# Kernel tuning notes

Measured on AMD Instinct MI355X. Metric: run time of the kernel, lower is better.

## Reference

```python
import jax, jax.numpy as jnp
import numpy as np

V = 50257
D = 512
T = 1024


def setup_inputs() -> dict:
    key = jax.random.key(0)
    ks = jax.random.split(key, 12)
    si = (2.0 / (V + D)) ** 0.5   # xavier-ish scale for input matrices
    sh = (1.0 / D) ** 0.5         # scale for recurrent matrices
    so = (2.0 / (V + D)) ** 0.5
    return {
        "idx": jax.random.randint(ks[0], (T,), 0, V, dtype=jnp.int32),
        "W_ii": jax.random.normal(ks[1], (D, V), jnp.float32) * si,
        "W_if": jax.random.normal(ks[2], (D, V), jnp.float32) * si,
        "W_io": jax.random.normal(ks[3], (D, V), jnp.float32) * si,
        "W_ig": jax.random.normal(ks[4], (D, V), jnp.float32) * si,
        "W_hi": jax.random.normal(ks[5], (D, D), jnp.float32) * sh,
        "W_hf": jax.random.normal(ks[6], (D, D), jnp.float32) * sh,
        "W_ho": jax.random.normal(ks[7], (D, D), jnp.float32) * sh,
        "W_hg": jax.random.normal(ks[8], (D, D), jnp.float32) * sh,
        "b_i": jnp.zeros((D,), jnp.float32),
        "b_f": jnp.ones((D,), jnp.float32),
        "b_o": jnp.zeros((D,), jnp.float32),
        "b_g": jnp.zeros((D,), jnp.float32),
        "W_out": jax.random.normal(ks[9], (V, D), jnp.float32) * so,
        "b_out": jnp.zeros((V,), jnp.float32),
    }


def reference(idx, W_ii, W_if, W_io, W_ig, W_hi, W_hf, W_ho, W_hg,
              b_i, b_f, b_o, b_g, W_out, b_out):
    # One-hot @ W.T == column gather: W[:, tok]. Dropout is identity (eval mode).
    dims = W_hi.shape[0]

    def step(carry, tok):
        h, c = carry
        i = jax.nn.sigmoid(W_ii[:, tok] + b_i + W_hi @ h)
        f = jax.nn.sigmoid(W_if[:, tok] + b_f + W_hf @ h)
        o = jax.nn.sigmoid(W_io[:, tok] + b_o + W_ho @ h)
        g = jnp.tanh(W_ig[:, tok] + b_g + W_hg @ h)
        c_new = f * c + i * g
        h_new = o * jnp.tanh(c_new)
        logits = W_out @ h_new + b_out          # [V]
        return (h_new, c_new), jax.nn.log_softmax(logits)

    h0 = jnp.zeros((dims,), W_hi.dtype)
    c0 = jnp.zeros((dims,), W_hi.dtype)
    (h, c), log_probs = jax.lax.scan(step, (h0, c0), idx)
    return log_probs, h, c  # log_probs: [T, V]
```

## Files before the change

### kernel.cpp

```cpp
#include <hip/hip_runtime.h>
#include <hip/hip_bf16.h>

#define VV 50257
#define DD 512
#define TT 1024
#define VPADN 50304
#define NBR 64
#define WCB 128
#define PSTR 400

typedef __bf16 bf16;
typedef __attribute__((ext_vector_type(8))) __bf16 bf16x8;
typedef __attribute__((ext_vector_type(4))) __bf16 bf16x4;
typedef __attribute__((ext_vector_type(4))) float f32x4;

__device__ __forceinline__ void gload_lds16(const void* g, void* l) {
  __builtin_amdgcn_global_load_lds(
      (__attribute__((address_space(1))) void*)(void*)g,
      (__attribute__((address_space(3))) void*)l, 16, 0, 0);
}

__global__ __launch_bounds__(512) __attribute__((amdgpu_waves_per_eu(2, 2)))
void recur_fused_kernel(
    const int* __restrict__ idx,
    const float* __restrict__ Wii, const float* __restrict__ Wif,
    const float* __restrict__ Wio, const float* __restrict__ Wig,
    const float* __restrict__ Whi, const float* __restrict__ Whf,
    const float* __restrict__ Who, const float* __restrict__ Whg,
    const float* __restrict__ bi, const float* __restrict__ bfv,
    const float* __restrict__ bo, const float* __restrict__ bg,
    const float* __restrict__ Wout,
    unsigned long long* __restrict__ Hpack, bf16* __restrict__ Hbf,
    bf16* __restrict__ Wbf, float* __restrict__ out_tail) {
  __shared__ float hsh[2][DD];
  __shared__ int idxs[TT];
  const int b = blockIdx.x, tid = threadIdx.x;

  if (b >= NBR) {
    const int wb = b - NBR;
    const size_t nch = (size_t)VPADN * DD / 4;
    for (size_t i = (size_t)wb * 512 + tid; i < nch; i += (size_t)WCB * 512) {
      size_t e = i << 2;
      bf16x4 o;
      if ((e >> 9) < VV) {
        f32x4 x = *(const f32x4*)&Wout[e];
        o[0] = (bf16)x[0]; o[1] = (bf16)x[1]; o[2] = (bf16)x[2]; o[3] = (bf16)x[3];
      } else {
        o[0] = o[1] = o[2] = o[3] = (bf16)0.f;
      }
      *(bf16x4*)&Wbf[e] = o;
    }
    return;
  }

  idxs[tid] = idx[tid];
  idxs[tid + 512] = idx[tid + 512];

  const int lane = tid & 63, w = tid >> 6;
  const int hd = (b << 3) + w;

  f32x4 wr0[4], wr1[4];
  {
    #pragma unroll
    for (int gg = 0; gg < 4; ++gg) {
      const float* Wg = (gg == 0) ? Whi : (gg == 1) ? Whf : (gg == 2) ? Who : Whg;
      wr0[gg] = *(const f32x4*)&Wg[(size_t)hd*DD + (lane << 2)];
      wr1[gg] = *(const f32x4*)&Wg[(size_t)hd*DD + 256 + (lane << 2)];
    }
  }
  #pragma unroll
  for (int gg = 0; gg < 4; ++gg) {
    asm volatile("" : "+v"(wr0[gg]));
    asm volatile("" : "+v"(wr1[gg]));
  }

  const float* wxp = nullptr;
  float bias = 0.f;
  if (lane < 4) {
    const float* Wx = (lane == 0) ? Wii : (lane == 1) ? Wif : (lane == 2) ? Wio : Wig;
    const float* bx = (lane == 0) ? bi : (lane == 1) ? bfv : (lane == 2) ? bo : bg;
    wxp = &Wx[(size_t)hd * VV];
    bias = bx[hd];
  }
  float c = 0.f, hout = 0.f;
  __syncthreads();

  for (int t = 0; t < TT; ++t) {
    float xv = 0.f;
    if (lane < 4) xv = wxp[idxs[t]] + bias;

    float* hb = hsh[t & 1];
    if (t > 0) {
      __builtin_amdgcn_s_sleep(8);
      const unsigned long long* src = &Hpack[(size_t)(t-1)*DD + tid];
      unsigned long long v;
      do {
        asm volatile("global_load_dwordx2 %0, %1, off sc1\n\t"
                     "s_waitcnt vmcnt(0)"
                     : "=v"(v) : "v"(src) : "memory");
      } while (__builtin_expect((unsigned)(v >> 32) != (unsigned)t, 0));
      hb[tid] = __uint_as_float((unsigned)v);
    } else {
      hb[tid] = 0.f;
    }
    __syncthreads();

    const f32x4 h0 = *(const f32x4*)&hb[lane << 2];
    const f32x4 h1 = *(const f32x4*)&hb[256 + (lane << 2)];
    f32x4 m0 = wr0[0]*h0 + wr1[0]*h1;
    f32x4 m1 = wr0[1]*h0 + wr1[1]*h1;
    f32x4 m2 = wr0[2]*h0 + wr1[2]*h1;
    f32x4 m3 = wr0[3]*h0 + wr1[3]*h1;
    float a0 = m0[0]+m0[1]+m0[2]+m0[3];
    float a1 = m1[0]+m1[1]+m1[2]+m1[3];
    float a2 = m2[0]+m2[1]+m2[2]+m2[3];
    float a3 = m3[0]+m3[1]+m3[2]+m3[3];
    #pragma unroll
    for (int mask = 1; mask < 64; mask <<= 1) {
      a0 += __shfl_xor(a0, mask);
      a1 += __shfl_xor(a1, mask);
      a2 += __shfl_xor(a2, mask);
      a3 += __shfl_xor(a3, mask);
    }

    float myacc = (lane == 0) ? a0 : (lane == 1) ? a1 : (lane == 2) ? a2 : a3;
    float pre = myacc + xv;
    bool isg = (lane == 3);
    float e1 = __expf(isg ? -2.f * pre : -pre);
    float rr = 1.f / (1.f + e1);
    float act = isg ? (2.f * rr - 1.f) : rr;

    float ia = __shfl(act, 0);
    float fa = __shfl(act, 1);
    float oa = __shfl(act, 2);
    float ga = __shfl(act, 3);

    if (lane == 0) {
      c = fa * c + ia * ga;
      float e2 = __expf(-2.f * c);
      float th = 2.f / (1.f + e2) - 1.f;
      hout = oa * th;
      unsigned long long pk =
          ((unsigned long long)(unsigned)(t + 1) << 32) |
          (unsigned long long)__float_as_uint(hout);
      __hip_atomic_store(&Hpack[(size_t)t*DD + hd], pk, __ATOMIC_RELAXED,
                         __HIP_MEMORY_SCOPE_AGENT);
      Hbf[(size_t)t*DD + hd] = (bf16)hout;
      if (t == TT - 1) { out_tail[hd] = hout; out_tail[DD + hd] = c; }
    }
  }
}

__global__ __launch_bounds__(256, 2) void gemm_kernel(
    const bf16* __restrict__ A, const bf16* __restrict__ B,
    const float* __restrict__ bout, float* __restrict__ Cout,
    float* __restrict__ Pmax, float* __restrict__ Psum) {
  __shared__ bf16 As[128*32];
  __shared__ bf16 Bs[128*32];
  __shared__ float Cs[4][16][72];
  __shared__ float partm[2][2][16];
  __shared__ float parts[2][2][16];
  const int tid = threadIdx.x;
  const int nb = blockIdx.x;
  const int n0 = nb * 128, m0 = blockIdx.y * 128;
  const int w = tid >> 6, l = tid & 63;
  const int wr = w >> 1, wc = w & 1;
  f32x4 acc[4][4] = {};

  for (int k0 = 0; k0 < DD; k0 += 32) {
    #pragma unroll
    for (int c = 0; c < 2; ++c) {
      int j = c*256 + tid;
      int row = j >> 2, kc = (j & 3) << 3;
      gload_lds16(&A[(size_t)(m0 + row)*DD + k0 + kc], (char*)As + (c*4096 + w*1024));
      gload_lds16(&B[(size_t)(n0 + row)*DD + k0 + kc], (char*)Bs + (c*4096 + w*1024));
    }
    __syncthreads();
    bf16x8 af[4], bfr[4];
    #pragma unroll
    for (int mi = 0; mi < 4; ++mi)
      af[mi] = *(const bf16x8*)&As[(wr*64 + mi*16 + (l & 15))*32 + (l >> 4)*8];
    #pragma unroll
    for (int ni = 0; ni < 4; ++ni)
      bfr[ni] = *(const bf16x8*)&Bs[(wc*64 + ni*16 + (l & 15))*32 + (l >> 4)*8];
    #pragma unroll
    for (int mi = 0; mi < 4; ++mi)
      #pragma unroll
      for (int ni = 0; ni < 4; ++ni)
        acc[mi][ni] = __builtin_amdgcn_mfma_f32_16x16x32_bf16(af[mi], bfr[ni], acc[mi][ni], 0, 0, 0);
    __syncthreads();
  }

  float bbv[4];
  bool colok[4];
  #pragma unroll
  for (int ni = 0; ni < 4; ++ni) {
    int col = n0 + wc*64 + ni*16 + (l & 15);
    colok[ni] = (col < VV);
    bbv[ni] = colok[ni] ? bout[col] : 0.f;
  }

  #pragma unroll
  for (int mi = 0; mi < 4; ++mi) {
    #pragma unroll
    for (int ni = 0; ni < 4; ++ni)
      #pragma unroll
      for (int r = 0; r < 4; ++r)
        Cs[w][(l >> 4)*4 + r][ni*16 + (l & 15)] = acc[mi][ni][r] + bbv[ni];

    #pragma unroll
    for (int r = 0; r < 4; ++r) {
      float v0 = colok[0] ? acc[mi][0][r] + bbv[0] : -1e30f;
      float v1 = colok[1] ? acc[mi][1][r] + bbv[1] : -1e30f;
      float v2 = colok[2] ? acc[mi][2][r] + bbv[2] : -1e30f;
      float v3 = colok[3] ? acc[mi][3][r] + bbv[3] : -1e30f;
      float pm = fmaxf(fmaxf(v0, v1), fmaxf(v2, v3));
      #pragma unroll
      for (int mk = 1; mk < 16; mk <<= 1) pm = fmaxf(pm, __shfl_xor(pm, mk));
      float ps = __expf(v0 - pm) + __expf(v1 - pm) + __expf(v2 - pm) + __expf(v3 - pm);
      #pragma unroll
      for (int mk = 1; mk < 16; mk <<= 1) ps += __shfl_xor(ps, mk);
      if ((l & 15) == 0) {
        partm[wr][wc][(l >> 4)*4 + r] = pm;
        parts[wr][wc][(l >> 4)*4 + r] = ps;
      }
    }
    __syncthreads();
    if (tid < 32) {
      int wr2 = tid >> 4, row16 = tid & 15;
      float ma = partm[wr2][0][row16], mb = partm[wr2][1][row16];
      float M = fmaxf(ma, mb);
      float S = parts[wr2][0][row16]*__expf(ma - M) + parts[wr2][1][row16]*__expf(mb - M);
      int gr = m0 + wr2*64 + mi*16 + row16;
      Pmax[(size_t)gr*PSTR + nb] = M;
      Psum[(size_t)gr*PSTR + nb] = S;
    }

    const int rbase = m0 + wr*64 + mi*16;
    #pragma unroll
    for (int i = 0; i < 4; ++i) {
      int idx2 = i*64 + l;
      int row = idx2 >> 4, quad = idx2 & 15;
      int col = n0 + wc*64 + quad*4;
      f32x4 v = *(const f32x4*)&Cs[w][row][quad*4];
      float* dst = &Cout[(size_t)(rbase + row)*VV + col];
      if (col + 3 < VV) {
        asm volatile("global_store_dwordx4 %0, %1, off"
                     :: "v"(dst), "v"(v) : "memory");
      } else {
        #pragma unroll
        for (int e = 0; e < 4; ++e)
          if (col + e < VV) dst[e] = v[e];
      }
    }
    __syncthreads();
  }
}

__global__ __launch_bounds__(512) void lsm_kernel(float* __restrict__ logits,
                                                  const float* __restrict__ Pmax,
                                                  const float* __restrict__ Psum) {
  const int t = blockIdx.x, tid = threadIdx.x;
  float* row = logits + (size_t)t*VV;

  float m = -1e30f, s = 0.f;
  if (tid < 393) {
    m = Pmax[(size_t)t*PSTR + tid];
    s = Psum[(size_t)t*PSTR + tid];
  }
  #pragma unroll
  for (int mask = 1; mask < 64; mask <<= 1) {
    float om = __shfl_xor(m, mask);
    float os = __shfl_xor(s, mask);
    float nm = fmaxf(m, om);
    s = s*__expf(m - nm) + os*__expf(om - nm);
    m = nm;
  }
  __shared__ float sm[8], ss[8], lse_sh;
  int wv = tid >> 6;
  if ((tid & 63) == 0) { sm[wv] = m; ss[wv] = s; }
  __syncthreads();
  if (tid == 0) {
    float M = sm[0], S = ss[0];
    for (int i2 = 1; i2 < 8; ++i2) {
      float nm = fmaxf(M, sm[i2]);
      S = S*__expf(M - nm) + ss[i2]*__expf(sm[i2] - nm);
      M = nm;
    }
    lse_sh = M + logf(S);
  }
  __syncthreads();
  const float lse = lse_sh;

  const size_t base = (size_t)t * VV;
  const int head = (int)((4 - (base & 3)) & 3);
  const int nvec = (VV - head) >> 2;
  const int tail0 = head + (nvec << 2);
  if (tid < head) row[tid] -= lse;
  else if (tid >= 508 && (tail0 + (tid - 508)) < VV) row[tail0 + (tid - 508)] -= lse;
  for (int i = tid; i < nvec; i += 512) {
    float* p = &row[head + (i << 2)];
    f32x4 x = *(const f32x4*)p;
    x[0] -= lse; x[1] -= lse; x[2] -= lse; x[3] -= lse;
    *(f32x4*)p = x;
  }
}

extern "C" void kernel_launch(void* const* d_in, const int* in_sizes, int n_in,
                              void* d_out, int out_size, void* d_ws, size_t ws_size,
                              hipStream_t stream) {
  const int*   idx  = (const int*)d_in[0];
  const float* Wii  = (const float*)d_in[1];
  const float* Wif  = (const float*)d_in[2];
  const float* Wio  = (const float*)d_in[3];
  const float* Wig  = (const float*)d_in[4];
  const float* Whi  = (const float*)d_in[5];
  const float* Whf  = (const float*)d_in[6];
  const float* Who  = (const float*)d_in[7];
  const float* Whg  = (const float*)d_in[8];
  const float* bi   = (const float*)d_in[9];
  const float* bfv  = (const float*)d_in[10];
  const float* bo   = (const float*)d_in[11];
  const float* bg   = (const float*)d_in[12];
  const float* Wout = (const float*)d_in[13];
  const float* bout = (const float*)d_in[14];
  float* out = (float*)d_out;

  char* ws = (char*)d_ws;
  bf16*  Wbf  = (bf16*)ws;
  unsigned long long* Hpack = (unsigned long long*)(ws + 51511296);
  bf16*  Hbf  = (bf16*)(ws + 55705600);
  float* Pmax = (float*)(ws + 56754176);
  float* Psum = (float*)(ws + 58392576);

  hipMemsetAsync(Hpack, 0, (size_t)TT*DD*8, stream);
  recur_fused_kernel<<<NBR + WCB, 512, 0, stream>>>(
      idx, Wii, Wif, Wio, Wig, Whi, Whf, Who, Whg, bi, bfv, bo, bg, Wout,
      Hpack, Hbf, Wbf, out + (size_t)TT*VV);
  gemm_kernel<<<dim3(393, 8), 256, 0, stream>>>(Hbf, Wbf, bout, out, Pmax, Psum);
  lsm_kernel<<<TT, 512, 0, stream>>>(out, Pmax, Psum);
}
```

Baseline: 2.127 ms.

## Fuse recurrence and output GEMM into one persistent kernel overlapping via flags

Merges the LSTM recurrence and the vocab-projection GEMM into a single launch. GEMM blocks spin on the packed step counter in Hpack until their 128 rows of h are ready, so the output projection overlaps the serial recurrence instead of waiting for it to finish. The separate Wout-to-bf16 conversion pass and the Hbf buffer are removed: the GEMM converts fp32 Wout and the packed h to bf16 on the fly while staging tiles to LDS. The GEMM tile becomes 128x256 with 512 threads, which halves the partial-softmax column count. The risks are spin-wait deadlock if GEMM blocks occupy the CUs before all recurrence blocks are resident, contention from polling traffic, and loss of async LDS loads.

```diff
diff --git a/kernel.cpp b/kernel.cpp
--- a/kernel.cpp
+++ b/kernel.cpp
@@ -4,24 +4,19 @@
 #define VV 50257
 #define DD 512
 #define TT 1024
-#define VPADN 50304
+#define NBLK 197
+#define PSTR 200
 #define NBR 64
-#define WCB 128
-#define PSTR 400
+#define GEMB (NBLK*8)
+#define TOTB (NBR + GEMB)
 
 typedef __bf16 bf16;
 typedef __attribute__((ext_vector_type(8))) __bf16 bf16x8;
-typedef __attribute__((ext_vector_type(4))) __bf16 bf16x4;
 typedef __attribute__((ext_vector_type(4))) float f32x4;
-
-__device__ __forceinline__ void gload_lds16(const void* g, void* l) {
-  __builtin_amdgcn_global_load_lds(
-      (__attribute__((address_space(1))) void*)(void*)g,
-      (__attribute__((address_space(3))) void*)l, 16, 0, 0);
-}
+typedef __attribute__((ext_vector_type(4))) unsigned int u32x4;
 
 __global__ __launch_bounds__(512) __attribute__((amdgpu_waves_per_eu(2, 2)))
-void recur_fused_kernel(
+void mega_kernel(
     const int* __restrict__ idx,
     const float* __restrict__ Wii, const float* __restrict__ Wif,
     const float* __restrict__ Wio, const float* __restrict__ Wig,
@@ -29,152 +24,191 @@
     const float* __restrict__ Who, const float* __restrict__ Whg,
     const float* __restrict__ bi, const float* __restrict__ bfv,
     const float* __restrict__ bo, const float* __restrict__ bg,
-    const float* __restrict__ Wout,
-    unsigned long long* __restrict__ Hpack, bf16* __restrict__ Hbf,
-    bf16* __restrict__ Wbf, float* __restrict__ out_tail) {
-  __shared__ float hsh[2][DD];
-  __shared__ int idxs[TT];
-  const int b = blockIdx.x, tid = threadIdx.x;
-
-  if (b >= NBR) {
-    const int wb = b - NBR;
-    const size_t nch = (size_t)VPADN * DD / 4;
-    for (size_t i = (size_t)wb * 512 + tid; i < nch; i += (size_t)WCB * 512) {
-      size_t e = i << 2;
-      bf16x4 o;
-      if ((e >> 9) < VV) {
-        f32x4 x = *(const f32x4*)&Wout[e];
-        o[0] = (bf16)x[0]; o[1] = (bf16)x[1]; o[2] = (bf16)x[2]; o[3] = (bf16)x[3];
-      } else {
-        o[0] = o[1] = o[2] = o[3] = (bf16)0.f;
-      }
-      *(bf16x4*)&Wbf[e] = o;
-    }
-    return;
-  }
-
-  idxs[tid] = idx[tid];
-  idxs[tid + 512] = idx[tid + 512];
-
-  const int lane = tid & 63, w = tid >> 6;
-  const int hd = (b << 3) + w;
-
-  f32x4 wr0[4], wr1[4];
-  {
+    const float* __restrict__ Wout, const float* __restrict__ bout,
+    unsigned long long* __restrict__ Hpack,
+    float* __restrict__ Cout, float* __restrict__ Pmax, float* __restrict__ Psum,
+    float* __restrict__ out_tail) {
+  __shared__ char smem[55296];
+  const int tid = threadIdx.x;
+
+  if (blockIdx.x < NBR) {
+    float (*hsh)[DD] = (float(*)[DD])smem;
+    int* idxs = (int*)(smem + 4096);
+    const int b = blockIdx.x;
+
+    idxs[tid] = idx[tid];
+    idxs[tid + 512] = idx[tid + 512];
+
+    const int lane = tid & 63, w = tid >> 6;
+    const int hd = (b << 3) + w;
+
+    f32x4 wr0[4], wr1[4];
     #pragma unroll
     for (int gg = 0; gg < 4; ++gg) {
       const float* Wg = (gg == 0) ? Whi : (gg == 1) ? Whf : (gg == 2) ? Who : Whg;
       wr0[gg] = *(const f32x4*)&Wg[(size_t)hd*DD + (lane << 2)];
       wr1[gg] = *(const f32x4*)&Wg[(size_t)hd*DD + 256 + (lane << 2)];
     }
-  }
-  #pragma unroll
-  for (int gg = 0; gg < 4; ++gg) {
-    asm volatile("" : "+v"(wr0[gg]));
-    asm volatile("" : "+v"(wr1[gg]));
-  }
-
-  const float* wxp = nullptr;
-  float bias = 0.f;
-  if (lane < 4) {
-    const float* Wx = (lane == 0) ? Wii : (lane == 1) ? Wif : (lane == 2) ? Wio : Wig;
-    const float* bx = (lane == 0) ? bi : (lane == 1) ? bfv : (lane == 2) ? bo : bg;
-    wxp = &Wx[(size_t)hd * VV];
-    bias = bx[hd];
-  }
-  float c = 0.f, hout = 0.f;
+    #pragma unroll
+    for (int gg = 0; gg < 4; ++gg) {
+      asm volatile("" : "+v"(wr0[gg]));
+      asm volatile("" : "+v"(wr1[gg]));
+    }
+
+    const float* wxp = nullptr;
+    float bias = 0.f;
+    if (lane < 4) {
+      const float* Wx = (lane == 0) ? Wii : (lane == 1) ? Wif : (lane == 2) ? Wio : Wig;
+      const float* bx = (lane == 0) ? bi : (lane == 1) ? bfv : (lane == 2) ? bo : bg;
+      wxp = &Wx[(size_t)hd * VV];
+      bias = bx[hd];
+    }
+    float c = 0.f, hout = 0.f;
+    __syncthreads();
+
+    for (int t = 0; t < TT; ++t) {
+      float xv = 0.f;
+      if (lane < 4) xv = wxp[idxs[t]] + bias;
+
+      float* hb = hsh[t & 1];
+      if (t > 0) {
+        const unsigned long long* src = &Hpack[(size_t)(t-1)*DD + tid];
+        unsigned long long v;
+        do {
+          asm volatile("global_load_dwordx2 %0, %1, off sc1\n\t"
+                       "s_waitcnt vmcnt(0)"
+                       : "=v"(v) : "v"(src) : "memory");
+        } while (__builtin_expect((unsigned)(v >> 32) != (unsigned)t, 0));
+        hb[tid] = __uint_as_float((unsigned)v);
+      } else {
+        hb[tid] = 0.f;
+      }
+      __syncthreads();
+
+      const f32x4 h0 = *(const f32x4*)&hb[lane << 2];
+      const f32x4 h1 = *(const f32x4*)&hb[256 + (lane << 2)];
+      f32x4 m0 = wr0[0]*h0 + wr1[0]*h1;
+      f32x4 m1 = wr0[1]*h0 + wr1[1]*h1;
+      f32x4 m2 = wr0[2]*h0 + wr1[2]*h1;
+      f32x4 m3 = wr0[3]*h0 + wr1[3]*h1;
+      float a0 = m0[0]+m0[1]+m0[2]+m0[3];
+      float a1 = m1[0]+m1[1]+m1[2]+m1[3];
+      float a2 = m2[0]+m2[1]+m2[2]+m2[3];
+      float a3 = m3[0]+m3[1]+m3[2]+m3[3];
+      #pragma unroll
+      for (int mask = 1; mask < 64; mask <<= 1) {
+        a0 += __shfl_xor(a0, mask);
+        a1 += __shfl_xor(a1, mask);
+        a2 += __shfl_xor(a2, mask);
+        a3 += __shfl_xor(a3, mask);
+      }
+
+      float myacc = (lane == 0) ? a0 : (lane == 1) ? a1 : (lane == 2) ? a2 : a3;
+      float pre = myacc + xv;
+      bool isg = (lane == 3);
+      float e1 = __expf(isg ? -2.f * pre : -pre);
+      float rr = 1.f / (1.f + e1);
+      float act = isg ? (2.f * rr - 1.f) : rr;
+
+      float ia = __shfl(act, 0);
+      float fa = __shfl(act, 1);
+      float oa = __shfl(act, 2);
+      float ga = __shfl(act, 3);
+
+      if (lane == 0) {
+        c = fa * c + ia * ga;
+        float e2 = __expf(-2.f * c);
+        float th = 2.f / (1.f + e2) - 1.f;
+        hout = oa * th;
+        unsigned long long pk =
+            ((unsigned long long)(unsigned)(t + 1) << 32) |
+            (unsigned long long)__float_as_uint(hout);
+        __hip_atomic_store(&Hpack[(size_t)t*DD + hd], pk, __ATOMIC_RELAXED,
+                           __HIP_MEMORY_SCOPE_AGENT);
+        if (t == TT - 1) { out_tail[hd] = hout; out_tail[DD + hd] = c; }
+      }
+    }
+    return;
+  }
+
+  bf16* As = (bf16*)smem;
+  bf16* Bs = (bf16*)(smem + 8192);
+  float (*Cs)[16][72] = (float(*)[16][72])smem;
+  float* partm = (float*)(smem + 36864);
+  float* parts = (float*)(smem + 37376);
+
+  const int gb = blockIdx.x - NBR;
+  const int my = gb / NBLK;
+  const int nb = gb % NBLK;
+  const int m0 = my << 7, n0 = nb << 8;
+  const int w = tid >> 6, l = tid & 63;
+  const int wr = w >> 2, wc = w & 3;
+
+  if (tid == 0) {
+    const unsigned long long* gp =
+        &Hpack[(size_t)(m0 + 127)*DD + ((unsigned)(nb*67 + my*13) & 511)];
+    for (;;) {
+      unsigned long long v = __hip_atomic_load(gp, __ATOMIC_RELAXED,
+                                               __HIP_MEMORY_SCOPE_AGENT);
+      if ((unsigned)(v >> 32) == (unsigned)(m0 + 128)) break;
+      __builtin_amdgcn_s_sleep(32);
+    }
+  }
   __syncthreads();
 
-  for (int t = 0; t < TT; ++t) {
-    float xv = 0.f;
-    if (lane < 4) xv = wxp[idxs[t]] + bias;
-
-    float* hb = hsh[t & 1];
-    if (t > 0) {
-      __builtin_amdgcn_s_sleep(8);
-      const unsigned long long* src = &Hpack[(size_t)(t-1)*DD + tid];
-      unsigned long long v;
-      do {
-        asm volatile("global_load_dwordx2 %0, %1, off sc1\n\t"
-                     "s_waitcnt vmcnt(0)"
-                     : "=v"(v) : "v"(src) : "memory");
-      } while (__builtin_expect((unsigned)(v >> 32) != (unsigned)t, 0));
-      hb[tid] = __uint_as_float((unsigned)v);
+  const int ar = tid >> 2;
+  const int ac = (tid & 3) << 3;
+  const unsigned expst = (unsigned)(m0 + ar + 1);
+  const unsigned long long* apb = &Hpack[(size_t)(m0 + ar)*DD + ac];
+  const int br = tid >> 1;
+  const int bc = (tid & 1) << 4;
+  const bool bok = (n0 + br) < VV;
+  const float* bpb = &Wout[(size_t)(n0 + br)*DD + bc];
+
+  f32x4 acc[4][4] = {};
+
+  for (int k0 = 0; k0 < DD; k0 += 32) {
+    u32x4 a0, a1, a2, a3;
+    const unsigned long long* ap = apb + k0;
+    for (;;) {
+      asm volatile("global_load_dwordx4 %0, %4, off sc1\n\t"
+                   "global_load_dwordx4 %1, %4, off offset:16 sc1\n\t"
+                   "global_load_dwordx4 %2, %4, off offset:32 sc1\n\t"
+                   "global_load_dwordx4 %3, %4, off offset:48 sc1\n\t"
+                   "s_waitcnt vmcnt(0)"
+                   : "=&v"(a0), "=&v"(a1), "=&v"(a2), "=&v"(a3)
+                   : "v"(ap) : "memory");
+      __builtin_amdgcn_sched_barrier(0);
+      if (a0[1] == expst && a0[3] == expst && a1[1] == expst && a1[3] == expst &&
+          a2[1] == expst && a2[3] == expst && a3[1] == expst && a3[3] == expst)
+        break;
+      __builtin_amdgcn_s_sleep(1);
+    }
+    bf16x8 av;
+    av[0] = (bf16)__uint_as_float(a0[0]); av[1] = (bf16)__uint_as_float(a0[2]);
+    av[2] = (bf16)__uint_as_float(a1[0]); av[3] = (bf16)__uint_as_float(a1[2]);
+    av[4] = (bf16)__uint_as_float(a2[0]); av[5] = (bf16)__uint_as_float(a2[2]);
+    av[6] = (bf16)__uint_as_float(a3[0]); av[7] = (bf16)__uint_as_float(a3[2]);
+    *(bf16x8*)&As[ar*32 + ac] = av;
+
+    bf16x8 bv0, bv1;
+    if (bok) {
+      const float* bp = bpb + k0;
+      f32x4 b0 = *(const f32x4*)bp;
+      f32x4 b1 = *(const f32x4*)(bp + 4);
+      f32x4 b2 = *(const f32x4*)(bp + 8);
+      f32x4 b3 = *(const f32x4*)(bp + 12);
+      bv0[0]=(bf16)b0[0]; bv0[1]=(bf16)b0[1]; bv0[2]=(bf16)b0[2]; bv0[3]=(bf16)b0[3];
+      bv0[4]=(bf16)b1[0]; bv0[5]=(bf16)b1[1]; bv0[6]=(bf16)b1[2]; bv0[7]=(bf16)b1[3];
+      bv1[0]=(bf16)b2[0]; bv1[1]=(bf16)b2[1]; bv1[2]=(bf16)b2[2]; bv1[3]=(bf16)b2[3];
+      bv1[4]=(bf16)b3[0]; bv1[5]=(bf16)b3[1]; bv1[6]=(bf16)b3[2]; bv1[7]=(bf16)b3[3];
     } else {
-      hb[tid] = 0.f;
-    }
-    __syncthreads();
-
-    const f32x4 h0 = *(const f32x4*)&hb[lane << 2];
-    const f32x4 h1 = *(const f32x4*)&hb[256 + (lane << 2)];
-    f32x4 m0 = wr0[0]*h0 + wr1[0]*h1;
-    f32x4 m1 = wr0[1]*h0 + wr1[1]*h1;
-    f32x4 m2 = wr0[2]*h0 + wr1[2]*h1;
-    f32x4 m3 = wr0[3]*h0 + wr1[3]*h1;
-    float a0 = m0[0]+m0[1]+m0[2]+m0[3];
-    float a1 = m1[0]+m1[1]+m1[2]+m1[3];
-    float a2 = m2[0]+m2[1]+m2[2]+m2[3];
-    float a3 = m3[0]+m3[1]+m3[2]+m3[3];
-    #pragma unroll
-    for (int mask = 1; mask < 64; mask <<= 1) {
-      a0 += __shfl_xor(a0, mask);
-      a1 += __shfl_xor(a1, mask);
-      a2 += __shfl_xor(a2, mask);
-      a3 += __shfl_xor(a3, mask);
-    }
-
-    float myacc = (lane == 0) ? a0 : (lane == 1) ? a1 : (lane == 2) ? a2 : a3;
-    float pre = myacc + xv;
-    bool isg = (lane == 3);
-    float e1 = __expf(isg ? -2.f * pre : -pre);
-    float rr = 1.f / (1.f + e1);
-    float act = isg ? (2.f * rr - 1.f) : rr;
-
-    float ia = __shfl(act, 0);
-    float fa = __shfl(act, 1);
-    float oa = __shfl(act, 2);
-    float ga = __shfl(act, 3);
-
-    if (lane == 0) {
-      c = fa * c + ia * ga;
-      float e2 = __expf(-2.f * c);
-      float th = 2.f / (1.f + e2) - 1.f;
-      hout = oa * th;
-      unsigned long long pk =
-          ((unsigned long long)(unsigned)(t + 1) << 32) |
-          (unsigned long long)__float_as_uint(hout);
-      __hip_atomic_store(&Hpack[(size_t)t*DD + hd], pk, __ATOMIC_RELAXED,
-                         __HIP_MEMORY_SCOPE_AGENT);
-      Hbf[(size_t)t*DD + hd] = (bf16)hout;
-      if (t == TT - 1) { out_tail[hd] = hout; out_tail[DD + hd] = c; }
-    }
-  }
-}
-
-__global__ __launch_bounds__(256, 2) void gemm_kernel(
-    const bf16* __restrict__ A, const bf16* __restrict__ B,
-    const float* __restrict__ bout, float* __restrict__ Cout,
-    float* __restrict__ Pmax, float* __restrict__ Psum) {
-  __shared__ bf16 As[128*32];
-  __shared__ bf16 Bs[128*32];
-  __shared__ float Cs[4][16][72];
-  __shared__ float partm[2][2][16];
-  __shared__ float parts[2][2][16];
-  const int tid = threadIdx.x;
-  const int nb = blockIdx.x;
-  const int n0 = nb * 128, m0 = blockIdx.y * 128;
-  const int w = tid >> 6, l = tid & 63;
-  const int wr = w >> 1, wc = w & 1;
-  f32x4 acc[4][4] = {};
-
-  for (int k0 = 0; k0 < DD; k0 += 32) {
-    #pragma unroll
-    for (int c = 0; c < 2; ++c) {
-      int j = c*256 + tid;
-      int row = j >> 2, kc = (j & 3) << 3;
-      gload_lds16(&A[(size_t)(m0 + row)*DD + k0 + kc], (char*)As + (c*4096 + w*1024));
-      gload_lds16(&B[(size_t)(n0 + row)*DD + k0 + kc], (char*)Bs + (c*4096 + w*1024));
-    }
+      #pragma unroll
+      for (int e = 0; e < 8; ++e) { bv0[e] = (bf16)0.f; bv1[e] = (bf16)0.f; }
+    }
+    *(bf16x8*)&Bs[br*32 + bc] = bv0;
+    *(bf16x8*)&Bs[br*32 + bc + 8] = bv1;
+
     __syncthreads();
     bf16x8 af[4], bfr[4];
     #pragma unroll
@@ -221,16 +255,22 @@
       #pragma unroll
       for (int mk = 1; mk < 16; mk <<= 1) ps += __shfl_xor(ps, mk);
       if ((l & 15) == 0) {
-        partm[wr][wc][(l >> 4)*4 + r] = pm;
-        parts[wr][wc][(l >> 4)*4 + r] = ps;
+        partm[(wr*4 + wc)*16 + (l >> 4)*4 + r] = pm;
+        parts[(wr*4 + wc)*16 + (l >> 4)*4 + r] = ps;
       }
     }
     __syncthreads();
     if (tid < 32) {
       int wr2 = tid >> 4, row16 = tid & 15;
-      float ma = partm[wr2][0][row16], mb = partm[wr2][1][row16];
-      float M = fmaxf(ma, mb);
-      float S = parts[wr2][0][row16]*__expf(ma - M) + parts[wr2][1][row16]*__expf(mb - M);
+      float M = -1e30f, S = 0.f;
+      #pragma unroll
+      for (int q = 0; q < 4; ++q) {
+        float mm = partm[(wr2*4 + q)*16 + row16];
+        float sp = parts[(wr2*4 + q)*16 + row16];
+        float nm = fmaxf(M, mm);
+        S = S*__expf(M - nm) + sp*__expf(mm - nm);
+        M = nm;
+      }
       int gr = m0 + wr2*64 + mi*16 + row16;
       Pmax[(size_t)gr*PSTR + nb] = M;
       Psum[(size_t)gr*PSTR + nb] = S;
@@ -264,7 +304,7 @@
   float* row = logits + (size_t)t*VV;
 
   float m = -1e30f, s = 0.f;
-  if (tid < 393) {
+  if (tid < NBLK) {
     m = Pmax[(size_t)t*PSTR + tid];
     s = Psum[(size_t)t*PSTR + tid];
   }
@@ -327,16 +367,13 @@
   float* out = (float*)d_out;
 
   char* ws = (char*)d_ws;
-  bf16*  Wbf  = (bf16*)ws;
-  unsigned long long* Hpack = (unsigned long long*)(ws + 51511296);
-  bf16*  Hbf  = (bf16*)(ws + 55705600);
-  float* Pmax = (float*)(ws + 56754176);
-  float* Psum = (float*)(ws + 58392576);
+  unsigned long long* Hpack = (unsigned long long*)ws;
+  float* Pmax = (float*)(ws + 4194304);
+  float* Psum = (float*)(ws + 5013504);
 
   hipMemsetAsync(Hpack, 0, (size_t)TT*DD*8, stream);
-  recur_fused_kernel<<<NBR + WCB, 512, 0, stream>>>(
-      idx, Wii, Wif, Wio, Wig, Whi, Whf, Who, Whg, bi, bfv, bo, bg, Wout,
-      Hpack, Hbf, Wbf, out + (size_t)TT*VV);
-  gemm_kernel<<<dim3(393, 8), 256, 0, stream>>>(Hbf, Wbf, bout, out, Pmax, Psum);
+  mega_kernel<<<TOTB, 512, 0, stream>>>(
+      idx, Wii, Wif, Wio, Wig, Whi, Whf, Who, Whg, bi, bfv, bo, bg, Wout, bout,
+      Hpack, out, Pmax, Psum, out + (size_t)TT*VV);
   lsm_kernel<<<TT, 512, 0, stream>>>(out, Pmax, Psum);
 }
```

Measured after the change: 1.950 ms (median of 3 runs). 1.09x faster.
